# Kernel optimization log

Measured on AMD Instinct MI355X. Metric: run time of the kernel, lower is better.

The kernel has to match this reference:

```python
import jax, jax.numpy as jnp
import numpy as np

B, S, H, NH = 8, 512, 4096, 64
HD = H // NH  # head dim = 64
LN_EPS = 1e-12
TOL_BITS = 16


def quant16(x):
    """Per-tensor dynamic fixed-point quantization to 16 bits.

    int_bit_width = ceil(log2(max|x|)) + 1 (sign bit); frac = 16 - int_bits.
    Values are rounded to the fixed-point grid and clipped to int16 range.
    """
    m = jnp.max(jnp.abs(x))
    int_bw = jnp.ceil(jnp.log2(jnp.maximum(m, 1e-12))) + 1.0
    frac_bw = jnp.asarray(TOL_BITS, x.dtype) - int_bw
    scale = jnp.exp2(frac_bw).astype(x.dtype)
    q = jnp.clip(jnp.round(x * scale), -32768.0, 32767.0) / scale
    return q


def setup_inputs() -> dict:
    key = jax.random.key(0)
    ks = jax.random.split(key, 6)
    s = 0.02
    return {
        "input_ids": jax.random.normal(ks[0], (B, S, H), jnp.float32),
        "attention_mask": jnp.zeros((B, 1, 1, S), jnp.float32),
        "Wq": jax.random.normal(ks[1], (H, H), jnp.float32) * s,
        "bq": jnp.zeros((H,), jnp.float32),
        "Wk": jax.random.normal(ks[2], (H, H), jnp.float32) * s,
        "bk": jnp.zeros((H,), jnp.float32),
        "Wv": jax.random.normal(ks[3], (H, H), jnp.float32) * s,
        "bv": jnp.zeros((H,), jnp.float32),
        "Wd": jax.random.normal(ks[4], (H, H), jnp.float32) * s,
        "bd": jnp.zeros((H,), jnp.float32),
        "ln_w": jnp.ones((H,), jnp.float32),
        "ln_b": jnp.zeros((H,), jnp.float32),
    }


def reference(input_ids, attention_mask, Wq, bq, Wk, bk, Wv, bv, Wd, bd, ln_w, ln_b):
    x = input_ids  # [B,S,H]
    # Q/K/V projections (torch Linear: y = x @ W.T + b), each followed by quant
    q = quant16(jnp.einsum('bsh,oh->bso', x, Wq) + bq)
    k = quant16(jnp.einsum('bsh,oh->bso', x, Wk) + bk)
    v = quant16(jnp.einsum('bsh,oh->bso', x, Wv) + bv)
    # split heads -> [B,NH,S,HD]
    q = q.reshape(B, S, NH, HD).transpose(0, 2, 1, 3)
    k = k.reshape(B, S, NH, HD).transpose(0, 2, 1, 3)
    v = v.reshape(B, S, NH, HD).transpose(0, 2, 1, 3)
    scores = jnp.einsum('bnqd,bnkd->bnqk', q, k) / np.sqrt(HD).astype(np.float32)
    scores = quant16(scores)
    scores = scores + attention_mask
    probs = jax.nn.softmax(scores, axis=-1)
    probs = quant16(probs)
    ctx = quant16(jnp.einsum('bnqk,bnkd->bnqd', probs, v))
    ctx = ctx.transpose(0, 2, 1, 3)  # [B,S,NH,HD]
    # dense: w = Wd.T reshaped to (NH, HD, H)
    w = Wd.T.reshape(NH, HD, H)
    proj = quant16(jnp.einsum('bfnd,ndh->bfh', ctx, w) + bd)
    # residual + LayerNorm
    y = x + proj
    mu = jnp.mean(y, axis=-1, keepdims=True)
    var = jnp.mean(jnp.square(y - mu), axis=-1, keepdims=True)
    y = (y - mu) / jnp.sqrt(var + LN_EPS) * ln_w + ln_b
    return quant16(y)
```

## Files before the change

kernel.cpp:

```cpp
#include <hip/hip_runtime.h>
#include <hip/hip_bf16.h>
#include <stdint.h>


typedef __attribute__((ext_vector_type(4))) float f32x4;
typedef __attribute__((ext_vector_type(8))) __bf16 bf16x8;

__device__ inline unsigned short f2bf(float f) {
  union { float f; unsigned u; } c; c.f = f;
  unsigned r = (c.u + 0x7fffu + ((c.u >> 16) & 1u)) >> 16;
  return (unsigned short)r;
}

__device__ inline void gload_lds16(const void* g, void* l) {
  __builtin_amdgcn_global_load_lds(
      (const __attribute__((address_space(1))) void*)g,
      (__attribute__((address_space(3))) void*)l, 16, 0, 0);
}

__global__ __launch_bounds__(256) void conv_all(
    const float* __restrict__ x, const float* __restrict__ wq,
    const float* __restrict__ wk, const float* __restrict__ wv,
    const float* __restrict__ wd, unsigned short* __restrict__ out) {
  int i = blockIdx.x * 256 + threadIdx.x;
  int reg = i >> 21;
  int off = i & 2097151;
  const float* src = (reg == 0) ? x : (reg == 1) ? wq : (reg == 2) ? wk
                     : (reg == 3) ? wv : wd;
  const float4* ip = (const float4*)src;
  float4 a = ip[off * 2], b = ip[off * 2 + 1];
  union { unsigned short s[8]; uint4 v; } o;
  o.s[0] = f2bf(a.x); o.s[1] = f2bf(a.y); o.s[2] = f2bf(a.z); o.s[3] = f2bf(a.w);
  o.s[4] = f2bf(b.x); o.s[5] = f2bf(b.y); o.s[6] = f2bf(b.z); o.s[7] = f2bf(b.w);
  ((uint4*)out)[i] = o.v;
}

template <int BIAS_MODE, int OUT_BF16>
__global__ __launch_bounds__(512, 2) void gemm_8p(
    const unsigned short* __restrict__ A, const unsigned short* __restrict__ Bw,
    const float* __restrict__ bias0, const float* __restrict__ bias1,
    const float* __restrict__ bias2, void* __restrict__ Cout,
    int M, int N, int K) {
  extern __shared__ unsigned short lds[];
  const int nbm = M >> 8, nbn = N >> 8, nwg = nbm * nbn;
  const int bid = blockIdx.x;
  const int wg = (bid & 7) * (nwg >> 3) + (bid >> 3);
  const int bm = wg % nbm, bn = wg / nbm;
  const int tid = threadIdx.x, w = tid >> 6, l = tid & 63;
  const int wr = w >> 2, wc = w & 3;
  const int lr = l & 15, lg = l >> 4;
  const unsigned short* gA = A + (size_t)bm * 256 * K;
  const unsigned short* gB = Bw + (size_t)bn * 256 * K;
  const int NT = K >> 6;
  const int srow = tid >> 3;
  const int scol = ((tid & 7) ^ (srow & 7)) << 3;
  f32x4 acc[8][4] = {};
  bf16x8 a[8], b[8];

#define STG(op, buf, h, kt)                                                    \
  {                                                                            \
    const unsigned short* g_ = (op) ? gB : gA;                                 \
    _Pragma("unroll")                                                          \
    for (int j_ = 0; j_ < 2; ++j_) {                                           \
      gload_lds16(                                                             \
          g_ + (size_t)((h) * 128 + j_ * 64 + srow) * K + (kt) * 64 + scol,    \
          &lds[((op) * 2 + (buf)) * 16384 + ((h) * 128 + j_ * 64) * 64 +       \
               w * 512]);                                                      \
    }                                                                          \
  }

#define RDA(buf, m, kk)                                                        \
  (*(const bf16x8*)&lds[(buf) * 16384 + (wr * 128 + (m) * 16 + lr) * 64 +      \
                        ((((kk) * 4 + lg) ^ (lr & 7)) << 3)])
#define RDB(buf, n, kk)                                                        \
  (*(const bf16x8*)&lds[(2 + (buf)) * 16384 + (wc * 64 + (n) * 16 + lr) * 64 + \
                        ((((kk) * 4 + lg) ^ (lr & 7)) << 3)])

#define LDA(buf, mh)                                                           \
  _Pragma("unroll")                                                            \
  for (int m_ = 0; m_ < 4; ++m_) {                                             \
    a[m_ * 2 + 0] = RDA(buf, (mh) * 4 + m_, 0);                                \
    a[m_ * 2 + 1] = RDA(buf, (mh) * 4 + m_, 1);                                \
  }
#define LDB(buf, nh)                                                           \
  _Pragma("unroll")                                                            \
  for (int n_ = 0; n_ < 2; ++n_) {                                             \
    b[((nh) * 2 + n_) * 2 + 0] = RDB(buf, (nh) * 2 + n_, 0);                   \
    b[((nh) * 2 + n_) * 2 + 1] = RDB(buf, (nh) * 2 + n_, 1);                   \
  }

#define MM(mbase, nbase)                                                       \
  __builtin_amdgcn_s_setprio(1);                                               \
  _Pragma("unroll")                                                            \
  for (int m_ = 0; m_ < 4; ++m_) {                                             \
    _Pragma("unroll")                                                          \
    for (int n_ = 0; n_ < 2; ++n_) {                                           \
      acc[(mbase) + m_][(nbase) + n_] =                                        \
          __builtin_amdgcn_mfma_f32_16x16x32_bf16(                             \
              a[m_ * 2], b[((nbase) + n_) * 2], acc[(mbase) + m_][(nbase) + n_],\
              0, 0, 0);                                                        \
      acc[(mbase) + m_][(nbase) + n_] =                                        \
          __builtin_amdgcn_mfma_f32_16x16x32_bf16(                             \
              a[m_ * 2 + 1], b[((nbase) + n_) * 2 + 1],                        \
              acc[(mbase) + m_][(nbase) + n_], 0, 0, 0);                       \
    }                                                                          \
  }                                                                            \
  __builtin_amdgcn_s_setprio(0);

#define BAR() __builtin_amdgcn_s_barrier()
#define VMW(n) asm volatile("s_waitcnt vmcnt(" #n ")" ::: "memory")

  STG(0, 0, 0, 0); STG(0, 0, 1, 0); STG(1, 0, 0, 0); STG(1, 0, 1, 0);
  STG(0, 1, 0, 1);
  VMW(2);
  BAR();

  const int NI = NT >> 1;
  for (int i = 0; i < NI; ++i) {
    const int t1 = 2 * i + 1, t2 = 2 * i + 2, t3 = 2 * i + 3;
    const bool s2 = t2 < NT, s3 = t3 < NT;
    LDA(0, 0); LDB(0, 0);
    STG(0, 1, 1, t1); STG(1, 1, 0, t1); STG(1, 1, 1, t1);
    BAR(); MM(0, 0); BAR();
    LDB(0, 1);
    BAR(); MM(0, 2); BAR();
    LDA(0, 1);
    BAR(); MM(4, 2); BAR();
    if (s2) { STG(0, 0, 0, t2); STG(0, 0, 1, t2); }
    BAR(); MM(4, 0);
    if (s2) VMW(4); else VMW(0);
    BAR();
    LDA(1, 0); LDB(1, 0);
    if (s2) { STG(1, 0, 0, t2); STG(1, 0, 1, t2); }
    BAR(); MM(0, 0); BAR();
    LDB(1, 1);
    BAR(); MM(0, 2); BAR();
    LDA(1, 1);
    BAR(); MM(4, 2); BAR();
    if (s3) STG(0, 1, 0, t3);
    BAR(); MM(4, 0);
    if (s3) VMW(2); else VMW(0);
    BAR();
  }

#pragma unroll
  for (int n = 0; n < 4; ++n) {
    int col = bn * 256 + wc * 64 + n * 16 + lr;
    float bv = 0.f;
    if (BIAS_MODE == 1) bv = bias0[col];
    else if (BIAS_MODE == 2)
      bv = (col < 4096) ? bias0[col] : (col < 8192 ? bias1[col - 4096] : bias2[col - 8192]);
#pragma unroll
    for (int m = 0; m < 8; ++m) {
#pragma unroll
      for (int r = 0; r < 4; ++r) {
        int row = bm * 256 + wr * 128 + m * 16 + lg * 4 + r;
        float v = acc[m][n][r] + bv;
        if (OUT_BF16)
          ((unsigned short*)Cout)[(size_t)row * N + col] = f2bf(v);
        else
          ((float*)Cout)[(size_t)row * N + col] = v;
      }
    }
  }
#undef STG
#undef RDA
#undef RDB
#undef LDA
#undef LDB
#undef MM
#undef BAR
#undef VMW
}

__global__ __launch_bounds__(512) void attn_kernel(
    const unsigned short* __restrict__ qkv, const float* __restrict__ mask,
    unsigned short* __restrict__ ctx) {
  extern __shared__ char smem[];
  unsigned short* Kt = (unsigned short*)smem;
  unsigned short* Vt = Kt + 512 * 64;
  unsigned short* Pb = Vt + 64 * 512;
  float* Mb = (float*)(Pb + 8 * 16 * 64);

  const int bid = blockIdx.x;
  const int b = bid >> 6, h = bid & 63;
  const int tid = threadIdx.x, w = tid >> 6, l = tid & 63;
  const size_t tokbase = (size_t)b * 512;

  Mb[tid < 512 ? tid : 0] = mask[b * 512 + (tid < 512 ? tid : 0)];
#pragma unroll
  for (int it = 0; it < 8; ++it) {
    int idx = it * 512 + tid;
    int row = idx >> 3, g = (idx & 7) << 3;
    const unsigned short* src = qkv + (tokbase + row) * 12288 + 4096 + h * 64 + g;
    uint4 v = *(const uint4*)src;
    *(uint4*)&Kt[row * 64 + (g ^ ((row & 7) << 3))] = v;
  }
#pragma unroll
  for (int it = 0; it < 8; ++it) {
    int idx = it * 512 + tid;
    int key = idx >> 3, g = (idx & 7) << 3;
    const unsigned short* src = qkv + (tokbase + key) * 12288 + 8192 + h * 64 + g;
    uint4 v = *(const uint4*)src;
    const unsigned short* e = (const unsigned short*)&v;
#pragma unroll
    for (int i = 0; i < 8; i++) {
      int d = g + i;
      Vt[d * 512 + (key ^ ((d & 7) << 3))] = e[i];
    }
  }
  __syncthreads();

  unsigned short* Pw = Pb + w * 16 * 64;
  const int lr = l & 15, lg = l >> 4;

  for (int c = 0; c < 4; ++c) {
    int q0 = w * 64 + c * 16;
    const unsigned short* qsrc = qkv + (tokbase + q0 + lr) * 12288 + h * 64 + lg * 8;
    bf16x8 qa0 = *(const bf16x8*)qsrc;
    bf16x8 qa1 = *(const bf16x8*)(qsrc + 32);
    f32x4 sc[32];
    f32x4 zero = {0.f, 0.f, 0.f, 0.f};
#pragma unroll
    for (int n = 0; n < 32; n++) {
      int key = n * 16 + lr;
      bf16x8 kb0 = *(const bf16x8*)&Kt[key * 64 + ((lg * 8) ^ ((key & 7) << 3))];
      bf16x8 kb1 = *(const bf16x8*)&Kt[key * 64 + ((32 + lg * 8) ^ ((key & 7) << 3))];
      f32x4 a = __builtin_amdgcn_mfma_f32_16x16x32_bf16(qa0, kb0, zero, 0, 0, 0);
      sc[n] = __builtin_amdgcn_mfma_f32_16x16x32_bf16(qa1, kb1, a, 0, 0, 0);
    }
    float rmax[4] = {-1e30f, -1e30f, -1e30f, -1e30f};
#pragma unroll
    for (int n = 0; n < 32; n++) {
      float mk = Mb[n * 16 + lr];
#pragma unroll
      for (int r = 0; r < 4; r++) {
        float s = sc[n][r] * 0.125f + mk;
        sc[n][r] = s;
        rmax[r] = fmaxf(rmax[r], s);
      }
    }
#pragma unroll
    for (int r = 0; r < 4; r++) {
      float m = rmax[r];
      m = fmaxf(m, __shfl_xor(m, 8)); m = fmaxf(m, __shfl_xor(m, 4));
      m = fmaxf(m, __shfl_xor(m, 2)); m = fmaxf(m, __shfl_xor(m, 1));
      rmax[r] = m;
    }
    float rsum[4] = {0.f, 0.f, 0.f, 0.f};
#pragma unroll
    for (int n = 0; n < 32; n++)
#pragma unroll
      for (int r = 0; r < 4; r++) {
        float p = __expf(sc[n][r] - rmax[r]);
        sc[n][r] = p;
        rsum[r] += p;
      }
#pragma unroll
    for (int r = 0; r < 4; r++) {
      float s = rsum[r];
      s += __shfl_xor(s, 8); s += __shfl_xor(s, 4);
      s += __shfl_xor(s, 2); s += __shfl_xor(s, 1);
      rsum[r] = s;
    }
    f32x4 cacc[4] = {};
#pragma unroll
    for (int kb = 0; kb < 8; ++kb) {
#pragma unroll
      for (int nn = 0; nn < 4; ++nn) {
        int colp = nn * 16 + lr;
#pragma unroll
        for (int r = 0; r < 4; r++) {
          int m = lg * 4 + r;
          Pw[m * 64 + (colp ^ ((m & 7) << 3))] = f2bf(sc[kb * 4 + nn][r]);
        }
      }
      bf16x8 pa0 = *(const bf16x8*)&Pw[lr * 64 + ((lg * 8) ^ ((lr & 7) << 3))];
      bf16x8 pa1 = *(const bf16x8*)&Pw[lr * 64 + ((32 + lg * 8) ^ ((lr & 7) << 3))];
#pragma unroll
      for (int dt = 0; dt < 4; ++dt) {
        int vr = dt * 16 + lr;
        int k0 = kb * 64 + lg * 8;
        bf16x8 vb0 = *(const bf16x8*)&Vt[vr * 512 + (k0 ^ ((vr & 7) << 3))];
        bf16x8 vb1 = *(const bf16x8*)&Vt[vr * 512 + ((k0 + 32) ^ ((vr & 7) << 3))];
        cacc[dt] = __builtin_amdgcn_mfma_f32_16x16x32_bf16(pa0, vb0, cacc[dt], 0, 0, 0);
        cacc[dt] = __builtin_amdgcn_mfma_f32_16x16x32_bf16(pa1, vb1, cacc[dt], 0, 0, 0);
      }
    }
#pragma unroll
    for (int dt = 0; dt < 4; ++dt)
#pragma unroll
      for (int r = 0; r < 4; r++) {
        int row = q0 + lg * 4 + r;
        float v = cacc[dt][r] / rsum[r];
        ctx[(tokbase + row) * 4096 + h * 64 + dt * 16 + lr] = f2bf(v);
      }
  }
}

__global__ __launch_bounds__(256) void ln_kernel(
    const float* __restrict__ x, float* __restrict__ io,
    const float* __restrict__ lnw, const float* __restrict__ lnb) {
  int t = blockIdx.x;
  const float4* xr = (const float4*)(x + (size_t)t * 4096);
  float4* pr = (float4*)(io + (size_t)t * 4096);
  float4 y[4];
  float sum = 0.f, sq = 0.f;
#pragma unroll
  for (int j = 0; j < 4; j++) {
    int i4 = j * 256 + threadIdx.x;
    float4 xv = xr[i4], pv = pr[i4];
    float4 yy;
    yy.x = xv.x + pv.x; yy.y = xv.y + pv.y; yy.z = xv.z + pv.z; yy.w = xv.w + pv.w;
    sum += yy.x + yy.y + yy.z + yy.w;
    sq += yy.x * yy.x + yy.y * yy.y + yy.z * yy.z + yy.w * yy.w;
    y[j] = yy;
  }
#pragma unroll
  for (int off = 32; off >= 1; off >>= 1) {
    sum += __shfl_down(sum, off);
    sq += __shfl_down(sq, off);
  }
  __shared__ float red[8];
  int w = threadIdx.x >> 6, l = threadIdx.x & 63;
  if (l == 0) { red[w] = sum; red[4 + w] = sq; }
  __syncthreads();
  float ts = red[0] + red[1] + red[2] + red[3];
  float tq = red[4] + red[5] + red[6] + red[7];
  float mean = ts * (1.f / 4096.f);
  float var = tq * (1.f / 4096.f) - mean * mean;
  float rs = rsqrtf(var + 1e-12f);
#pragma unroll
  for (int j = 0; j < 4; j++) {
    int i4 = j * 256 + threadIdx.x;
    float4 wv = ((const float4*)lnw)[i4];
    float4 bb = ((const float4*)lnb)[i4];
    float4 o;
    o.x = (y[j].x - mean) * rs * wv.x + bb.x;
    o.y = (y[j].y - mean) * rs * wv.y + bb.y;
    o.z = (y[j].z - mean) * rs * wv.z + bb.z;
    o.w = (y[j].w - mean) * rs * wv.w + bb.w;
    pr[i4] = o;
  }
}

extern "C" void kernel_launch(void* const* d_in, const int* in_sizes, int n_in,
                              void* d_out, int out_size, void* d_ws, size_t ws_size,
                              hipStream_t stream) {
  const float* x   = (const float*)d_in[0];
  const float* msk = (const float*)d_in[1];
  const float* Wq  = (const float*)d_in[2];
  const float* bq  = (const float*)d_in[3];
  const float* Wk  = (const float*)d_in[4];
  const float* bk  = (const float*)d_in[5];
  const float* Wv  = (const float*)d_in[6];
  const float* bv  = (const float*)d_in[7];
  const float* Wd  = (const float*)d_in[8];
  const float* bd  = (const float*)d_in[9];
  const float* lnw = (const float*)d_in[10];
  const float* lnb = (const float*)d_in[11];
  float* out = (float*)d_out;

  unsigned short* xb    = (unsigned short*)d_ws;
  unsigned short* wqkvb = xb + (size_t)16777216;
  unsigned short* wdb   = wqkvb + (size_t)50331648;
  unsigned short* qkvb  = wdb + (size_t)16777216;
  unsigned short* ctxb  = wqkvb;

  conv_all<<<40960, 256, 0, stream>>>(x, Wq, Wk, Wv, Wd, xb);

  (void)hipFuncSetAttribute((const void*)(gemm_8p<2, 1>),
                            hipFuncAttributeMaxDynamicSharedMemorySize, 131072);
  (void)hipFuncSetAttribute((const void*)(gemm_8p<1, 0>),
                            hipFuncAttributeMaxDynamicSharedMemorySize, 131072);

  gemm_8p<2, 1><<<768, 512, 131072, stream>>>(xb, wqkvb, bq, bk, bv, qkvb,
                                              4096, 12288, 4096);

  (void)hipFuncSetAttribute((const void*)attn_kernel,
                            hipFuncAttributeMaxDynamicSharedMemorySize, 149504);
  attn_kernel<<<512, 512, 149504, stream>>>(qkvb, msk, ctxb);

  gemm_8p<1, 0><<<256, 512, 131072, stream>>>(ctxb, wdb, bd, nullptr, nullptr,
                                              out, 4096, 4096, 4096);

  ln_kernel<<<4096, 256, 0, stream>>>(x, out, lnw, lnb);
}
```

Baseline: 774.5 us.

## Restructure GEMM main loop from eight to four phases per iteration

The bf16 GEMM main loop is rescheduled from an 8-phase ping-pong to a 4-phase one. Each phase now issues more LDS reads and two MFMA blocks between barriers, and the global-to-LDS staging order and vmcnt waits are changed to match. This halves the number of barriers per K-tile pair and cuts synchronisation overhead. In exchange it interleaves loads and MFMAs less finely and raises register pressure from holding more fragments at once.

```diff
diff --git a/kernel.cpp b/kernel.cpp
--- a/kernel.cpp
+++ b/kernel.cpp
@@ -36,7 +36,7 @@
 }
 
 template <int BIAS_MODE, int OUT_BF16>
-__global__ __launch_bounds__(512, 2) void gemm_8p(
+__global__ __launch_bounds__(512, 2) void gemm_4p(
     const unsigned short* __restrict__ A, const unsigned short* __restrict__ Bw,
     const float* __restrict__ bias0, const float* __restrict__ bias1,
     const float* __restrict__ bias2, void* __restrict__ Cout,
@@ -108,38 +108,33 @@
   __builtin_amdgcn_s_setprio(0);
 
 #define BAR() __builtin_amdgcn_s_barrier()
-#define VMW(n) asm volatile("s_waitcnt vmcnt(" #n ")" ::: "memory")
+#define VMW4() asm volatile("s_waitcnt vmcnt(4)" ::: "memory")
+#define VMW0() asm volatile("s_waitcnt vmcnt(0)" ::: "memory")
 
   STG(0, 0, 0, 0); STG(0, 0, 1, 0); STG(1, 0, 0, 0); STG(1, 0, 1, 0);
-  STG(0, 1, 0, 1);
-  VMW(2);
+  STG(1, 1, 0, 1); STG(1, 1, 1, 1);
+  VMW4();
   BAR();
 
   const int NI = NT >> 1;
   for (int i = 0; i < NI; ++i) {
     const int t1 = 2 * i + 1, t2 = 2 * i + 2, t3 = 2 * i + 3;
     const bool s2 = t2 < NT, s3 = t3 < NT;
-    LDA(0, 0); LDB(0, 0);
-    STG(0, 1, 1, t1); STG(1, 1, 0, t1); STG(1, 1, 1, t1);
-    BAR(); MM(0, 0); BAR();
-    LDB(0, 1);
-    BAR(); MM(0, 2); BAR();
+    LDA(0, 0); LDB(0, 0); LDB(0, 1);
+    STG(0, 1, 0, t1); STG(0, 1, 1, t1);
+    BAR(); MM(0, 0); MM(0, 2); BAR();
     LDA(0, 1);
-    BAR(); MM(4, 2); BAR();
+    if (s2) { STG(1, 0, 0, t2); STG(1, 0, 1, t2); }
+    BAR(); MM(4, 0); MM(4, 2);
+    if (s2) VMW4(); else VMW0();
+    BAR();
+    LDA(1, 0); LDB(1, 0); LDB(1, 1);
     if (s2) { STG(0, 0, 0, t2); STG(0, 0, 1, t2); }
-    BAR(); MM(4, 0);
-    if (s2) VMW(4); else VMW(0);
-    BAR();
-    LDA(1, 0); LDB(1, 0);
-    if (s2) { STG(1, 0, 0, t2); STG(1, 0, 1, t2); }
-    BAR(); MM(0, 0); BAR();
-    LDB(1, 1);
-    BAR(); MM(0, 2); BAR();
+    BAR(); MM(0, 0); MM(0, 2); BAR();
     LDA(1, 1);
-    BAR(); MM(4, 2); BAR();
-    if (s3) STG(0, 1, 0, t3);
-    BAR(); MM(4, 0);
-    if (s3) VMW(2); else VMW(0);
+    if (s3) { STG(1, 1, 0, t3); STG(1, 1, 1, t3); }
+    BAR(); MM(4, 0); MM(4, 2);
+    if (s3) VMW4(); else VMW0();
     BAR();
   }
 
@@ -170,7 +165,8 @@
 #undef LDB
 #undef MM
 #undef BAR
-#undef VMW
+#undef VMW4
+#undef VMW0
 }
 
 __global__ __launch_bounds__(512) void attn_kernel(
@@ -369,19 +365,19 @@
 
   conv_all<<<40960, 256, 0, stream>>>(x, Wq, Wk, Wv, Wd, xb);
 
-  (void)hipFuncSetAttribute((const void*)(gemm_8p<2, 1>),
+  (void)hipFuncSetAttribute((const void*)(gemm_4p<2, 1>),
                             hipFuncAttributeMaxDynamicSharedMemorySize, 131072);
-  (void)hipFuncSetAttribute((const void*)(gemm_8p<1, 0>),
+  (void)hipFuncSetAttribute((const void*)(gemm_4p<1, 0>),
                             hipFuncAttributeMaxDynamicSharedMemorySize, 131072);
 
-  gemm_8p<2, 1><<<768, 512, 131072, stream>>>(xb, wqkvb, bq, bk, bv, qkvb,
+  gemm_4p<2, 1><<<768, 512, 131072, stream>>>(xb, wqkvb, bq, bk, bv, qkvb,
                                               4096, 12288, 4096);
 
   (void)hipFuncSetAttribute((const void*)attn_kernel,
                             hipFuncAttributeMaxDynamicSharedMemorySize, 149504);
   attn_kernel<<<512, 512, 149504, stream>>>(qkvb, msk, ctxb);
 
-  gemm_8p<1, 0><<<256, 512, 131072, stream>>>(ctxb, wdb, bd, nullptr, nullptr,
+  gemm_4p<1, 0><<<256, 512, 131072, stream>>>(ctxb, wdb, bd, nullptr, nullptr,
                                               out, 4096, 4096, 4096);
 
   ln_kernel<<<4096, 256, 0, stream>>>(x, out, lnw, lnb);
```

Result: faster. 759.1 us (-2.0%).
